# Kernel optimization log

Measured on AMD Instinct MI355X. Metric: run time of the kernel, lower is better.

## Reference

```python
import jax, jax.numpy as jnp
import numpy as np

B, N, DIM, H = 8, 4096, 768, 12
HD = DIM // H
SCALE = HD ** -0.5


def setup_inputs() -> dict:
    key = jax.random.key(0)
    ks = jax.random.split(key, 6)
    x = jax.random.normal(ks[0], (B, N, DIM), dtype=jnp.float32)
    # torch nn.Linear weights: [out_features, in_features]
    Wqkv = jax.random.normal(ks[1], (3 * DIM, DIM), dtype=jnp.float32) * (DIM ** -0.5)
    Wp = jax.random.normal(ks[2], (DIM, DIM), dtype=jnp.float32) * (DIM ** -0.5)
    bp = jnp.zeros((DIM,), dtype=jnp.float32)
    w_q = jax.random.normal(ks[3], (H, HD), dtype=jnp.float32)
    w_k = jax.random.normal(ks[4], (H, HD), dtype=jnp.float32)
    return {"x": x, "Wqkv": Wqkv, "Wp": Wp, "bp": bp, "w_q": w_q, "w_k": w_k}


def reference(x, Wqkv, Wp, bp, w_q, w_k):
    b, n, c = x.shape
    qkv = x @ Wqkv.T                                   # [B,N,3C]
    # rearrange 'B N (qkv H C) -> qkv B H N C'
    qkv = qkv.reshape(b, n, 3, H, HD).transpose(2, 0, 3, 1, 4)
    q, k, v = qkv[0], qkv[1], qkv[2]                   # each [B,H,N,hd]

    alpha = jnp.einsum('bhnc,hc->bhn', q, w_q) * SCALE
    alpha = jax.nn.softmax(alpha, axis=-1)             # [B,H,N]
    global_q = jnp.einsum('bhn,bhnc->bhc', alpha, q)   # [B,H,hd]

    p = global_q[:, :, None, :] * k                    # [B,H,N,hd]
    beta = jnp.einsum('bhnc,hc->bhn', p, w_k) * SCALE
    beta = jax.nn.softmax(beta, axis=-1)
    global_k = jnp.einsum('bhn,bhnc->bhc', beta, k)    # [B,H,hd]

    u = global_k[:, :, None, :] * v                    # [B,H,N,hd]
    q_flat = q.transpose(0, 2, 1, 3).reshape(b, n, c)  # 'B H N C -> B N (H C)'
    u_flat = u.transpose(0, 2, 1, 3).reshape(b, n, c)
    return u_flat @ Wp.T + bp + q_flat
```

## Files before the change

### kernel.cpp

```cpp
#include <hip/hip_runtime.h>
#include <hip/hip_bf16.h>
#include <cstdint>
#include <cstddef>

#define B_ 8
#define N_ 4096
#define DIM_ 768
#define H_ 12
#define M_ (B_*N_)
#define SCALE_ 0.125f
#define NS2 16
#define KDIM 768
#define NKT 12
#define NITER 6
#define QKS 1536

typedef __attribute__((ext_vector_type(8))) short s8v;
typedef __attribute__((ext_vector_type(4))) float f4v;

__device__ inline float bf2f(unsigned short u) {
    unsigned v = ((unsigned)u) << 16;
    return __builtin_bit_cast(float, v);
}
__device__ inline unsigned short f2bf(float f) {
    unsigned u = __builtin_bit_cast(unsigned, f);
    return (unsigned short)((u + 0x7FFFu + ((u >> 16) & 1u)) >> 16);
}
__device__ inline void gload16(const void* g, void* l) {
    __builtin_amdgcn_global_load_lds(
        (const __attribute__((address_space(1))) void*)g,
        (__attribute__((address_space(3))) void*)l, 16, 0, 0);
}

#define BARX() __builtin_amdgcn_s_barrier()
#define PRIO1() __builtin_amdgcn_s_setprio(1)
#define PRIO0() __builtin_amdgcn_s_setprio(0)
#define VM4() asm volatile("s_waitcnt vmcnt(4)" ::: "memory")
#define VM0() asm volatile("s_waitcnt vmcnt(0)" ::: "memory")

template<int EPI>
__global__ __launch_bounds__(512, 2)
void gemm8(const unsigned short* __restrict__ A, int ldaE,
           const unsigned short* __restrict__ Bmat,
           unsigned short* __restrict__ Cb,
           int Nc, int ntn)
{
    __shared__ __align__(16) char smem[131072];
    const int tid = threadIdx.x;
    const int l = tid & 63, w = tid >> 6;
    const int lr = l & 15, g = l >> 4;
    const int wm = w >> 2, wn = w & 3;

    const int nwg = gridDim.x, cpx = nwg >> 3;
    const int bid = blockIdx.x;
    int lg = (bid & 7) * cpx + (bid >> 3);

    size_t batch_off = 0;
    if (EPI == 2) {
        const int bb = lg / 9;
        lg -= bb * 9;
        batch_off = (size_t)bb * (DIM_ * DIM_);
    }
    const int tm = lg / ntn, tn = lg % ntn;
    const int m0 = tm * 256, n0 = tn * 256;

    const long ldaB = (long)ldaE * 2;
    const long ldbB = (long)KDIM * 2;

    const int srA = w * 8 + (l >> 3);
    const int kbs = (l & 7) * 16;
    const int kbx = kbs ^ ((srA & 7) << 4);
    long offA[2], offB[2];
    offA[0] = (long)(srA) * ldaB + kbx;
    offA[1] = (long)(128 + srA) * ldaB + kbx;
    offB[0] = (long)(((srA >> 5)) * 64 + (srA & 31)) * ldbB + kbx;
    offB[1] = (long)((2 + (srA >> 5)) * 64 + (srA & 31)) * ldbB + kbx;

    const char* Abase = (const char*)(A + batch_off + (size_t)m0 * ldaE);
    const char* Bbase = (const char*)(Bmat + (size_t)n0 * KDIM);

    const int aoff = (wm * 64 + lr) * 128;
    const int boff = (wn * 32 + lr) * 128;
    const int kx0 = (g * 16) ^ ((lr & 7) << 4);
    const int kx1 = (64 + g * 16) ^ ((lr & 7) << 4);

    f4v acc[8][4] = {};
    s8v af[4][2];
    s8v bfr[2][2][2];

#define STG_A(buf_, qm_, kt_) { \
    const char* s0_ = Abase + (long)(kt_) * 2 + (long)(qm_) * 64 * ldaB; \
    char* d0_ = smem + ((buf_) * 4 + (qm_)) * 16384 + w * 1024; \
    gload16(s0_ + offA[0], d0_); \
    gload16(s0_ + offA[1], d0_ + 8192); }

#define STG_B(buf_, qn_, kt_) { \
    const char* s0_ = Bbase + (long)(kt_) * 2 + (long)(qn_) * 32 * ldbB; \
    char* d0_ = smem + ((buf_) * 4 + 2 + (qn_)) * 16384 + w * 1024; \
    gload16(s0_ + offB[0], d0_); \
    gload16(s0_ + offB[1], d0_ + 8192); }

#define DS_A(buf_, qm_) { \
    const char* ba_ = smem + ((buf_) * 4 + (qm_)) * 16384 + aoff; \
    af[0][0] = *(const s8v*)(ba_ +    0 + kx0); af[0][1] = *(const s8v*)(ba_ +    0 + kx1); \
    af[1][0] = *(const s8v*)(ba_ + 2048 + kx0); af[1][1] = *(const s8v*)(ba_ + 2048 + kx1); \
    af[2][0] = *(const s8v*)(ba_ + 4096 + kx0); af[2][1] = *(const s8v*)(ba_ + 4096 + kx1); \
    af[3][0] = *(const s8v*)(ba_ + 6144 + kx0); af[3][1] = *(const s8v*)(ba_ + 6144 + kx1); }

#define DS_B(buf_, qn_) { \
    const char* bb_ = smem + ((buf_) * 4 + 2 + (qn_)) * 16384 + boff; \
    bfr[qn_][0][0] = *(const s8v*)(bb_ +    0 + kx0); bfr[qn_][0][1] = *(const s8v*)(bb_ +    0 + kx1); \
    bfr[qn_][1][0] = *(const s8v*)(bb_ + 2048 + kx0); bfr[qn_][1][1] = *(const s8v*)(bb_ + 2048 + kx1); }

#define MM(fmg_, fng_, qn_, kk_) \
    acc[fmg_][fng_] = __builtin_amdgcn_mfma_f32_16x16x32_bf16(af[(fmg_)&3][kk_], bfr[qn_][(fng_)&1][kk_], acc[fmg_][fng_], 0, 0, 0);

#define MFMA8(qm_, qn_, kk_) \
    MM((qm_)*4+0, (qn_)*2+0, qn_, kk_) MM((qm_)*4+0, (qn_)*2+1, qn_, kk_) \
    MM((qm_)*4+1, (qn_)*2+0, qn_, kk_) MM((qm_)*4+1, (qn_)*2+1, qn_, kk_) \
    MM((qm_)*4+2, (qn_)*2+0, qn_, kk_) MM((qm_)*4+2, (qn_)*2+1, qn_, kk_) \
    MM((qm_)*4+3, (qn_)*2+0, qn_, kk_) MM((qm_)*4+3, (qn_)*2+1, qn_, kk_)

#define MFMA16(qm_, qn_) { MFMA8(qm_, qn_, 0) MFMA8(qm_, qn_, 1) }

    STG_A(0, 0, 0); STG_B(0, 0, 0); STG_A(0, 1, 0); STG_B(0, 1, 0);
    STG_A(1, 0, 64); STG_B(1, 0, 64);
    VM4(); BARX();

    for (int i = 0; i < NITER; ++i) {
        const int t1k = (2 * i + 1) * 64, t2k = (2 * i + 2) * 64, t3k = (2 * i + 3) * 64;
        const bool h2 = (2 * i + 2) < NKT, h3 = (2 * i + 3) < NKT;
        const bool last = (i == NITER - 1);
        DS_A(0, 0); DS_B(0, 0); STG_B(1, 1, t1k);
        BARX(); PRIO1(); MFMA16(0, 0); PRIO0(); BARX();
        DS_B(0, 1); STG_A(1, 1, t1k);
        BARX(); PRIO1(); MFMA16(0, 1); PRIO0(); BARX();
        DS_A(0, 1); if (h2) STG_A(0, 0, t2k);
        BARX(); PRIO1(); MFMA16(1, 0); PRIO0(); BARX();
        if (h2) STG_B(0, 0, t2k);
        BARX(); PRIO1(); MFMA16(1, 1); PRIO0();
        if (last) { VM0(); } else { VM4(); }
        BARX();
        DS_A(1, 0); DS_B(1, 0); if (h2) STG_A(0, 1, t2k);
        BARX(); PRIO1(); MFMA16(0, 0); PRIO0(); BARX();
        DS_B(1, 1); if (h2) STG_B(0, 1, t2k);
        BARX(); PRIO1(); MFMA16(0, 1); PRIO0(); BARX();
        DS_A(1, 1); if (h3) STG_A(1, 0, t3k);
        BARX(); PRIO1(); MFMA16(1, 0); PRIO0(); BARX();
        if (h3) STG_B(1, 0, t3k);
        BARX(); PRIO1(); MFMA16(1, 1); PRIO0();
        if (last) { VM0(); } else { VM4(); }
        BARX();
    }

#pragma unroll
    for (int fmg = 0; fmg < 8; ++fmg) {
#pragma unroll
        for (int fng = 0; fng < 4; ++fng) {
            const int col = n0 + wn * 64 + fng * 16 + lr;
#pragma unroll
            for (int r = 0; r < 4; ++r) {
                const int row = m0 + wm * 128 + fmg * 16 + g * 4 + r;
                Cb[batch_off + (size_t)row * Nc + col] = f2bf(acc[fmg][fng][r]);
            }
        }
    }
#undef STG_A
#undef STG_B
#undef DS_A
#undef DS_B
#undef MM
#undef MFMA8
#undef MFMA16
}

__global__ __launch_bounds__(512, 2)
void gemm128_epi(const unsigned short* __restrict__ A, int ldaE,
                 const unsigned short* __restrict__ Bmat,
                 float* __restrict__ Cf,
                 const float* __restrict__ bias, const unsigned short* __restrict__ Qf,
                 int Nc, int ntn)
{
    __shared__ __align__(16) char smem[98304];
    const int tid = threadIdx.x;
    const int l = tid & 63, w = tid >> 6;
    const int lr = l & 15, g = l >> 4;
    const int wm = w >> 2, wn = w & 3;

    const int nwg = gridDim.x, cpx = nwg >> 3;
    const int bid = blockIdx.x;
    const int lg = (bid & 7) * cpx + (bid >> 3);
    const int tm = lg / ntn, tn = lg % ntn;
    const int m0 = tm * 128, n0 = tn * 256;

    const long ldaB = (long)ldaE * 2;
    const long ldbB = (long)KDIM * 2;

    const unsigned short* Bp = Bmat + (size_t)(m0 >> 12) * (DIM_ * DIM_);

    const int srA = w * 8 + (l >> 3);
    const int kbs = (l & 7) * 16;
    const int kbx = kbs ^ ((srA & 7) << 4);
    long offA[2], offB[2];
    offA[0] = (long)(srA) * ldaB + kbx;
    offA[1] = (long)(64 + srA) * ldaB + kbx;
    offB[0] = (long)(((srA >> 5)) * 64 + (srA & 31)) * ldbB + kbx;
    offB[1] = (long)((2 + (srA >> 5)) * 64 + (srA & 31)) * ldbB + kbx;

    const char* Abase = (const char*)(A + (size_t)m0 * ldaE);
    const char* Bbase = (const char*)(Bp + (size_t)n0 * KDIM);

    const int aoff = (wm * 64 + lr) * 128;
    const int boff = (wn * 32 + lr) * 128;
    const int kx0 = (g * 16) ^ ((lr & 7) << 4);
    const int kx1 = (64 + g * 16) ^ ((lr & 7) << 4);

    f4v acc[4][4] = {};
    s8v af[4][2];
    s8v bfr[2][2][2];

#define STG_A1(buf_, kt_) { \
    const char* s0_ = Abase + (long)(kt_) * 2; \
    char* d0_ = smem + ((buf_) * 3) * 16384 + w * 1024; \
    gload16(s0_ + offA[0], d0_); \
    gload16(s0_ + offA[1], d0_ + 8192); }

#define STG_B1(buf_, qn_, kt_) { \
    const char* s0_ = Bbase + (long)(kt_) * 2 + (long)(qn_) * 32 * ldbB; \
    char* d0_ = smem + ((buf_) * 3 + 1 + (qn_)) * 16384 + w * 1024; \
    gload16(s0_ + offB[0], d0_); \
    gload16(s0_ + offB[1], d0_ + 8192); }

#define DS_A1(buf_) { \
    const char* ba_ = smem + ((buf_) * 3) * 16384 + aoff; \
    af[0][0] = *(const s8v*)(ba_ +    0 + kx0); af[0][1] = *(const s8v*)(ba_ +    0 + kx1); \
    af[1][0] = *(const s8v*)(ba_ + 2048 + kx0); af[1][1] = *(const s8v*)(ba_ + 2048 + kx1); \
    af[2][0] = *(const s8v*)(ba_ + 4096 + kx0); af[2][1] = *(const s8v*)(ba_ + 4096 + kx1); \
    af[3][0] = *(const s8v*)(ba_ + 6144 + kx0); af[3][1] = *(const s8v*)(ba_ + 6144 + kx1); }

#define DS_B1(buf_, qn_) { \
    const char* bb_ = smem + ((buf_) * 3 + 1 + (qn_)) * 16384 + boff; \
    bfr[qn_][0][0] = *(const s8v*)(bb_ +    0 + kx0); bfr[qn_][0][1] = *(const s8v*)(bb_ +    0 + kx1); \
    bfr[qn_][1][0] = *(const s8v*)(bb_ + 2048 + kx0); bfr[qn_][1][1] = *(const s8v*)(bb_ + 2048 + kx1); }

#define MM1(fm_, fng_, qn_, kk_) \
    acc[fm_][fng_] = __builtin_amdgcn_mfma_f32_16x16x32_bf16(af[fm_][kk_], bfr[qn_][(fng_)&1][kk_], acc[fm_][fng_], 0, 0, 0);

#define MFMA16_1(qn_, kk_) \
    MM1(0, (qn_)*2+0, qn_, kk_) MM1(0, (qn_)*2+1, qn_, kk_) \
    MM1(1, (qn_)*2+0, qn_, kk_) MM1(1, (qn_)*2+1, qn_, kk_) \
    MM1(2, (qn_)*2+0, qn_, kk_) MM1(2, (qn_)*2+1, qn_, kk_) \
    MM1(3, (qn_)*2+0, qn_, kk_) MM1(3, (qn_)*2+1, qn_, kk_)

#define MFMA32_1(qn_) { MFMA16_1(qn_, 0) MFMA16_1(qn_, 1) }

    STG_A1(0, 0); STG_B1(0, 0, 0); STG_B1(0, 1, 0);
    STG_A1(1, 64); STG_B1(1, 0, 64);
    VM4(); BARX();

    for (int i = 0; i < NITER; ++i) {
        const int t1k = (2 * i + 1) * 64, t2k = (2 * i + 2) * 64, t3k = (2 * i + 3) * 64;
        const bool h2 = (2 * i + 2) < NKT, h3 = (2 * i + 3) < NKT;
        const bool last = (i == NITER - 1);
        DS_A1(0); DS_B1(0, 0); STG_B1(1, 1, t1k);
        BARX(); PRIO1(); MFMA32_1(0); PRIO0(); BARX();
        DS_B1(0, 1); if (h2) { STG_A1(0, t2k); STG_B1(0, 0, t2k); }
        BARX(); PRIO1(); MFMA32_1(1); PRIO0();
        if (last) { VM0(); } else { VM4(); }
        BARX();
        DS_A1(1); DS_B1(1, 0); if (h2) STG_B1(0, 1, t2k);
        BARX(); PRIO1(); MFMA32_1(0); PRIO0(); BARX();
        DS_B1(1, 1); if (h3) { STG_A1(1, t3k); STG_B1(1, 0, t3k); }
        BARX(); PRIO1(); MFMA32_1(1); PRIO0();
        if (last) { VM0(); } else { VM4(); }
        BARX();
    }

#pragma unroll
    for (int fm = 0; fm < 4; ++fm) {
#pragma unroll
        for (int fng = 0; fng < 4; ++fng) {
            const int col = n0 + wn * 64 + fng * 16 + lr;
#pragma unroll
            for (int r = 0; r < 4; ++r) {
                const int row = m0 + wm * 64 + fm * 16 + g * 4 + r;
                Cf[(size_t)row * Nc + col] = acc[fm][fng][r] + bias[col]
                                             + bf2f(Qf[(size_t)row * QKS + col]);
            }
        }
    }
#undef STG_A1
#undef STG_B1
#undef DS_A1
#undef DS_B1
#undef MM1
#undef MFMA16_1
#undef MFMA32_1
}

__global__ __launch_bounds__(256)
void fused_path(const unsigned short* __restrict__ qkv, int col_off,
                const float* __restrict__ vec, int per_bh,
                float* __restrict__ partv, float* __restrict__ partms)
{
    const int bid = blockIdx.x;
    const int bh = bid / NS2, sp = bid % NS2;
    const int b = bh / H_, h = bh % H_;
    const int t = threadIdx.x;
    const int lane8 = t & 7, grp = t >> 3;

    const unsigned short* base = qkv + ((size_t)(b * N_ + sp * 256) * QKS)
                                 + col_off + h * 64 + lane8 * 8;
    const float* wv = vec + (per_bh ? bh * 64 : h * 64) + lane8 * 8;
    float w8[8];
#pragma unroll
    for (int j = 0; j < 8; j++) w8[j] = wv[j];

    float q[8][8];
    float d[8];
#pragma unroll
    for (int pass = 0; pass < 8; ++pass) {
        const int row = pass * 32 + grp;
        s8v q8 = *(const s8v*)(base + (size_t)row * QKS);
        float s = 0.f;
#pragma unroll
        for (int j = 0; j < 8; j++) {
            q[pass][j] = bf2f((unsigned short)q8[j]);
            s += q[pass][j] * w8[j];
        }
        s += __shfl_xor(s, 1); s += __shfl_xor(s, 2); s += __shfl_xor(s, 4);
        d[pass] = s * SCALE_;
    }
    float m = d[0];
#pragma unroll
    for (int pass = 1; pass < 8; ++pass) m = fmaxf(m, d[pass]);
    float ssum = 0.f;
    float a8[8] = {};
#pragma unroll
    for (int pass = 0; pass < 8; ++pass) {
        float e = __expf(d[pass] - m);
        ssum += e;
#pragma unroll
        for (int j = 0; j < 8; j++) a8[j] += e * q[pass][j];
    }

    __shared__ float Lm[32], Ls[32];
    __shared__ float La[32][64];
    if (lane8 == 0) { Lm[grp] = m; Ls[grp] = ssum; }
#pragma unroll
    for (int j = 0; j < 8; j++) La[grp][lane8 * 8 + j] = a8[j];
    __syncthreads();

    if (t < 64) {
        float mstar = Lm[0];
#pragma unroll
        for (int g2 = 1; g2 < 32; ++g2) mstar = fmaxf(mstar, Lm[g2]);
        float sstar = 0.f, v = 0.f;
#pragma unroll
        for (int g2 = 0; g2 < 32; ++g2) {
            float e = __expf(Lm[g2] - mstar);
            sstar += Ls[g2] * e;
            v += La[g2][t] * e;
        }
        partv[(size_t)bid * 64 + t] = v;
        if (t == 0) { partms[bid * 2] = mstar; partms[bid * 2 + 1] = sstar; }
    }
}

__global__ void path_reduce(const float* __restrict__ partv, const float* __restrict__ partms,
                            float* __restrict__ gout,
                            const float* __restrict__ wk, float* __restrict__ bvec)
{
    const int bh = blockIdx.x;
    const int t = threadIdx.x;
    const int h = bh % H_;
    float mstar = partms[(bh * NS2) * 2];
#pragma unroll
    for (int p = 1; p < NS2; ++p) mstar = fmaxf(mstar, partms[(bh * NS2 + p) * 2]);
    float sstar = 0.f, v = 0.f;
#pragma unroll
    for (int p = 0; p < NS2; ++p) {
        float e = __expf(partms[(bh * NS2 + p) * 2] - mstar);
        sstar += partms[(bh * NS2 + p) * 2 + 1] * e;
        v += partv[(size_t)(bh * NS2 + p) * 64 + t] * e;
    }
    float g = v / sstar;
    gout[bh * 64 + t] = g;
    if (wk) bvec[bh * 64 + t] = g * wk[h * 64 + t];
}

__global__ void cvt_all(const float* __restrict__ x, const float* __restrict__ Wqkv,
                        unsigned short* __restrict__ xb, unsigned short* __restrict__ wqkb,
                        unsigned short* __restrict__ wvT,
                        int n4x, int n4xw)
{
    int i = blockIdx.x * 256 + threadIdx.x;
    if (i < n4xw) {
        const float* src; unsigned short* dst; int k;
        if (i < n4x) { src = x; dst = xb; k = i; }
        else { src = Wqkv; dst = wqkb; k = i - n4x; }
        float4 v = ((const float4*)src)[k];
        ushort4 o;
        o.x = f2bf(v.x); o.y = f2bf(v.y); o.z = f2bf(v.z); o.w = f2bf(v.w);
        ((ushort4*)dst)[k] = o;
    } else {
        const int k = i - n4xw;
        const int ii = k % DIM_;
        const int c0 = (k / DIM_) * 4;
        ushort4 o;
        o.x = f2bf(Wqkv[(size_t)(2 * DIM_ + c0 + 0) * DIM_ + ii]);
        o.y = f2bf(Wqkv[(size_t)(2 * DIM_ + c0 + 1) * DIM_ + ii]);
        o.z = f2bf(Wqkv[(size_t)(2 * DIM_ + c0 + 2) * DIM_ + ii]);
        o.w = f2bf(Wqkv[(size_t)(2 * DIM_ + c0 + 3) * DIM_ + ii]);
        *(ushort4*)&wvT[(size_t)ii * DIM_ + c0] = o;
    }
}

__global__ __launch_bounds__(256)
void fold_wp(const float* __restrict__ Wp, const float* __restrict__ gk,
             unsigned short* __restrict__ W2)
{
    int idx = blockIdx.x * 256 + threadIdx.x;
    int e4 = idx * 4;
    int b = (int)((unsigned)e4 / (unsigned)(DIM_ * DIM_));
    int rem = e4 - b * (DIM_ * DIM_);
    int c = rem % DIM_;
    float4 wv = *(const float4*)&Wp[rem];
    const float* gp = &gk[b * DIM_ + c];
    ushort4 o;
    o.x = f2bf(wv.x * gp[0]); o.y = f2bf(wv.y * gp[1]);
    o.z = f2bf(wv.z * gp[2]); o.w = f2bf(wv.w * gp[3]);
    *(ushort4*)&W2[e4] = o;
}

extern "C" void kernel_launch(void* const* d_in, const int* in_sizes, int n_in,
                              void* d_out, int out_size, void* d_ws, size_t ws_size,
                              hipStream_t stream)
{
    const float* x    = (const float*)d_in[0];
    const float* Wqkv = (const float*)d_in[1];
    const float* Wp   = (const float*)d_in[2];
    const float* bp   = (const float*)d_in[3];
    const float* w_q  = (const float*)d_in[4];
    const float* w_k  = (const float*)d_in[5];
    float* out = (float*)d_out;

    constexpr size_t NXB  = (size_t)M_ * DIM_;
    constexpr size_t NWQK = (size_t)2 * DIM_ * DIM_;
    constexpr size_t NWV  = (size_t)DIM_ * DIM_;
    constexpr size_t NQK  = (size_t)M_ * QKS;
    constexpr size_t NW2  = (size_t)B_ * DIM_ * DIM_;

    char* p = (char*)d_ws;
    unsigned short* xb    = (unsigned short*)p; p += NXB * 2;
    unsigned short* wqkb  = (unsigned short*)p; p += NWQK * 2;
    unsigned short* wvT   = (unsigned short*)p; p += NWV * 2;
    unsigned short* qkb   = (unsigned short*)p; p += NQK * 2;
    unsigned short* w2b   = (unsigned short*)p; p += NW2 * 2;
    unsigned short* w3b   = (unsigned short*)p; p += NW2 * 2;
    float* pv1  = (float*)p; p += (size_t)B_ * H_ * NS2 * 64 * 4;
    float* pms1 = (float*)p; p += (size_t)B_ * H_ * NS2 * 2 * 4;
    float* gq   = (float*)p; p += (size_t)B_ * H_ * 64 * 4;
    float* bvec = (float*)p; p += (size_t)B_ * H_ * 64 * 4;
    float* gkv  = (float*)p; p += (size_t)B_ * H_ * 64 * 4;

    constexpr int N4X  = (int)(NXB / 4);
    constexpr int N4XW = N4X + (int)(NWQK / 4);
    constexpr int NTOT = N4XW + (int)(NWV / 4);
    cvt_all<<<NTOT / 256, 256, 0, stream>>>(x, Wqkv, xb, wqkb, wvT, N4X, N4XW);

    gemm8<0><<<128 * 6, 512, 0, stream>>>(xb, DIM_, wqkb, qkb, QKS, 6);

    fused_path<<<B_ * H_ * NS2, 256, 0, stream>>>(qkb, 0, w_q, 0, pv1, pms1);
    path_reduce<<<B_ * H_, 64, 0, stream>>>(pv1, pms1, gq, w_k, bvec);

    fused_path<<<B_ * H_ * NS2, 256, 0, stream>>>(qkb, DIM_, bvec, 1, pv1, pms1);
    path_reduce<<<B_ * H_, 64, 0, stream>>>(pv1, pms1, gkv, nullptr, nullptr);

    fold_wp<<<(int)(NW2 / 4 / 256), 256, 0, stream>>>(Wp, gkv, w2b);

    gemm8<2><<<72, 512, 0, stream>>>(w2b, DIM_, wvT, w3b, DIM_, 3);

    gemm128_epi<<<256 * 3, 512, 0, stream>>>(xb, DIM_, w3b, out, bp, qkb, DIM_, 3);
}
```

Before: 223.3 us.

## Fuse alpha-softmax partial reduction into QKV GEMM epilogue and retile weight-fold GEMM

The QKV GEMM epilogue now computes the per-head q·w_q logits, a local max, exp-sum and the weighted q partial sums directly from the accumulators. It writes 32 partial slices per (batch, head), which removes the separate fused_path pass that re-read Q from memory. path_reduce now takes the partial count as a runtime argument. The batched Wp-fold × WvT GEMM moves from a 72-block 256-tile kernel to a 144-block 128-row-tile variant to use more CUs. The cost is extra shuffles and register pressure in the big GEMM's epilogue.

```diff
diff --git a/kernel.cpp b/kernel.cpp
--- a/kernel.cpp
+++ b/kernel.cpp
@@ -38,11 +38,12 @@
 #define VM4() asm volatile("s_waitcnt vmcnt(4)" ::: "memory")
 #define VM0() asm volatile("s_waitcnt vmcnt(0)" ::: "memory")
 
-template<int EPI>
 __global__ __launch_bounds__(512, 2)
 void gemm8(const unsigned short* __restrict__ A, int ldaE,
            const unsigned short* __restrict__ Bmat,
            unsigned short* __restrict__ Cb,
+           const float* __restrict__ w_q,
+           float* __restrict__ pv1, float* __restrict__ pms1,
            int Nc, int ntn)
 {
     __shared__ __align__(16) char smem[131072];
@@ -53,14 +54,7 @@
 
     const int nwg = gridDim.x, cpx = nwg >> 3;
     const int bid = blockIdx.x;
-    int lg = (bid & 7) * cpx + (bid >> 3);
-
-    size_t batch_off = 0;
-    if (EPI == 2) {
-        const int bb = lg / 9;
-        lg -= bb * 9;
-        batch_off = (size_t)bb * (DIM_ * DIM_);
-    }
+    const int lg = (bid & 7) * cpx + (bid >> 3);
     const int tm = lg / ntn, tn = lg % ntn;
     const int m0 = tm * 256, n0 = tn * 256;
 
@@ -76,7 +70,7 @@
     offB[0] = (long)(((srA >> 5)) * 64 + (srA & 31)) * ldbB + kbx;
     offB[1] = (long)((2 + (srA >> 5)) * 64 + (srA & 31)) * ldbB + kbx;
 
-    const char* Abase = (const char*)(A + batch_off + (size_t)m0 * ldaE);
+    const char* Abase = (const char*)(A + (size_t)m0 * ldaE);
     const char* Bbase = (const char*)(Bmat + (size_t)n0 * KDIM);
 
     const int aoff = (wm * 64 + lr) * 128;
@@ -161,7 +155,66 @@
 #pragma unroll
             for (int r = 0; r < 4; ++r) {
                 const int row = m0 + wm * 128 + fmg * 16 + g * 4 + r;
-                Cb[batch_off + (size_t)row * Nc + col] = f2bf(acc[fmg][fng][r]);
+                Cb[(size_t)row * Nc + col] = f2bf(acc[fmg][fng][r]);
+            }
+        }
+    }
+
+    if (tn < 3) {
+        const int h = tn * 4 + wn;
+        float wq[4];
+#pragma unroll
+        for (int f = 0; f < 4; ++f) wq[f] = w_q[h * 64 + f * 16 + lr];
+
+        float d[8][4];
+#pragma unroll
+        for (int fmg = 0; fmg < 8; ++fmg) {
+#pragma unroll
+            for (int r = 0; r < 4; ++r) {
+                float s = acc[fmg][0][r] * wq[0] + acc[fmg][1][r] * wq[1]
+                        + acc[fmg][2][r] * wq[2] + acc[fmg][3][r] * wq[3];
+                s += __shfl_xor(s, 1); s += __shfl_xor(s, 2);
+                s += __shfl_xor(s, 4); s += __shfl_xor(s, 8);
+                d[fmg][r] = s * SCALE_;
+            }
+        }
+        float mw = d[0][0];
+#pragma unroll
+        for (int fmg = 0; fmg < 8; ++fmg)
+#pragma unroll
+            for (int r = 0; r < 4; ++r) mw = fmaxf(mw, d[fmg][r]);
+        mw = fmaxf(mw, __shfl_xor(mw, 16));
+        mw = fmaxf(mw, __shfl_xor(mw, 32));
+
+        float ssum = 0.f;
+        float pvec[4] = {};
+#pragma unroll
+        for (int fmg = 0; fmg < 8; ++fmg) {
+#pragma unroll
+            for (int r = 0; r < 4; ++r) {
+                const float e = __expf(d[fmg][r] - mw);
+                ssum += e;
+#pragma unroll
+                for (int f = 0; f < 4; ++f) pvec[f] += e * acc[fmg][f][r];
+            }
+        }
+        ssum += __shfl_xor(ssum, 16); ssum += __shfl_xor(ssum, 32);
+#pragma unroll
+        for (int f = 0; f < 4; ++f) {
+            pvec[f] += __shfl_xor(pvec[f], 16);
+            pvec[f] += __shfl_xor(pvec[f], 32);
+        }
+
+        const int b = m0 >> 12;
+        const int bh = b * H_ + h;
+        const int slice = ((m0 & (N_ - 1)) >> 7) + wm;
+        if (g == 0) {
+#pragma unroll
+            for (int f = 0; f < 4; ++f)
+                pv1[(size_t)(bh * 32 + slice) * 64 + f * 16 + lr] = pvec[f];
+            if (lr == 0) {
+                pms1[(bh * 32 + slice) * 2] = mw;
+                pms1[(bh * 32 + slice) * 2 + 1] = ssum;
             }
         }
     }
@@ -174,12 +227,13 @@
 #undef MFMA16
 }
 
+template<int MODE>
 __global__ __launch_bounds__(512, 2)
-void gemm128_epi(const unsigned short* __restrict__ A, int ldaE,
-                 const unsigned short* __restrict__ Bmat,
-                 float* __restrict__ Cf,
-                 const float* __restrict__ bias, const unsigned short* __restrict__ Qf,
-                 int Nc, int ntn)
+void gemm128(const unsigned short* __restrict__ A, int ldaE,
+             const unsigned short* __restrict__ Bmat,
+             float* __restrict__ Cf, unsigned short* __restrict__ CbO,
+             const float* __restrict__ bias, const unsigned short* __restrict__ Qf,
+             int Nc, int ntn)
 {
     __shared__ __align__(16) char smem[98304];
     const int tid = threadIdx.x;
@@ -196,7 +250,8 @@
     const long ldaB = (long)ldaE * 2;
     const long ldbB = (long)KDIM * 2;
 
-    const unsigned short* Bp = Bmat + (size_t)(m0 >> 12) * (DIM_ * DIM_);
+    const unsigned short* Bp = Bmat;
+    if (MODE == 0) Bp = Bmat + (size_t)(m0 >> 12) * (DIM_ * DIM_);
 
     const int srA = w * 8 + (l >> 3);
     const int kbs = (l & 7) * 16;
@@ -284,8 +339,12 @@
 #pragma unroll
             for (int r = 0; r < 4; ++r) {
                 const int row = m0 + wm * 64 + fm * 16 + g * 4 + r;
-                Cf[(size_t)row * Nc + col] = acc[fm][fng][r] + bias[col]
-                                             + bf2f(Qf[(size_t)row * QKS + col]);
+                if (MODE == 0) {
+                    Cf[(size_t)row * Nc + col] = acc[fm][fng][r] + bias[col]
+                                                 + bf2f(Qf[(size_t)row * QKS + col]);
+                } else {
+                    CbO[(size_t)row * Nc + col] = f2bf(acc[fm][fng][r]);
+                }
             }
         }
     }
@@ -368,21 +427,19 @@
 }
 
 __global__ void path_reduce(const float* __restrict__ partv, const float* __restrict__ partms,
-                            float* __restrict__ gout,
+                            int nsp, float* __restrict__ gout,
                             const float* __restrict__ wk, float* __restrict__ bvec)
 {
     const int bh = blockIdx.x;
     const int t = threadIdx.x;
     const int h = bh % H_;
-    float mstar = partms[(bh * NS2) * 2];
-#pragma unroll
-    for (int p = 1; p < NS2; ++p) mstar = fmaxf(mstar, partms[(bh * NS2 + p) * 2]);
+    float mstar = partms[(bh * nsp) * 2];
+    for (int p = 1; p < nsp; ++p) mstar = fmaxf(mstar, partms[(bh * nsp + p) * 2]);
     float sstar = 0.f, v = 0.f;
-#pragma unroll
-    for (int p = 0; p < NS2; ++p) {
-        float e = __expf(partms[(bh * NS2 + p) * 2] - mstar);
-        sstar += partms[(bh * NS2 + p) * 2 + 1] * e;
-        v += partv[(size_t)(bh * NS2 + p) * 64 + t] * e;
+    for (int p = 0; p < nsp; ++p) {
+        float e = __expf(partms[(bh * nsp + p) * 2] - mstar);
+        sstar += partms[(bh * nsp + p) * 2 + 1] * e;
+        v += partv[(size_t)(bh * nsp + p) * 64 + t] * e;
     }
     float g = v / sstar;
     gout[bh * 64 + t] = g;
@@ -458,8 +515,10 @@
     unsigned short* qkb   = (unsigned short*)p; p += NQK * 2;
     unsigned short* w2b   = (unsigned short*)p; p += NW2 * 2;
     unsigned short* w3b   = (unsigned short*)p; p += NW2 * 2;
-    float* pv1  = (float*)p; p += (size_t)B_ * H_ * NS2 * 64 * 4;
-    float* pms1 = (float*)p; p += (size_t)B_ * H_ * NS2 * 2 * 4;
+    float* pv1  = (float*)p; p += (size_t)B_ * H_ * 32 * 64 * 4;
+    float* pms1 = (float*)p; p += (size_t)B_ * H_ * 32 * 2 * 4;
+    float* pv2  = (float*)p; p += (size_t)B_ * H_ * NS2 * 64 * 4;
+    float* pms2 = (float*)p; p += (size_t)B_ * H_ * NS2 * 2 * 4;
     float* gq   = (float*)p; p += (size_t)B_ * H_ * 64 * 4;
     float* bvec = (float*)p; p += (size_t)B_ * H_ * 64 * 4;
     float* gkv  = (float*)p; p += (size_t)B_ * H_ * 64 * 4;
@@ -469,17 +528,17 @@
     constexpr int NTOT = N4XW + (int)(NWV / 4);
     cvt_all<<<NTOT / 256, 256, 0, stream>>>(x, Wqkv, xb, wqkb, wvT, N4X, N4XW);
 
-    gemm8<0><<<128 * 6, 512, 0, stream>>>(xb, DIM_, wqkb, qkb, QKS, 6);
-
-    fused_path<<<B_ * H_ * NS2, 256, 0, stream>>>(qkb, 0, w_q, 0, pv1, pms1);
-    path_reduce<<<B_ * H_, 64, 0, stream>>>(pv1, pms1, gq, w_k, bvec);
-
-    fused_path<<<B_ * H_ * NS2, 256, 0, stream>>>(qkb, DIM_, bvec, 1, pv1, pms1);
-    path_reduce<<<B_ * H_, 64, 0, stream>>>(pv1, pms1, gkv, nullptr, nullptr);
+    gemm8<<<128 * 6, 512, 0, stream>>>(xb, DIM_, wqkb, qkb, w_q, pv1, pms1, QKS, 6);
+
+    path_reduce<<<B_ * H_, 64, 0, stream>>>(pv1, pms1, 32, gq, w_k, bvec);
+
+    fused_path<<<B_ * H_ * NS2, 256, 0, stream>>>(qkb, DIM_, bvec, 1, pv2, pms2);
+    path_reduce<<<B_ * H_, 64, 0, stream>>>(pv2, pms2, NS2, gkv, nullptr, nullptr);
 
     fold_wp<<<(int)(NW2 / 4 / 256), 256, 0, stream>>>(Wp, gkv, w2b);
 
-    gemm8<2><<<72, 512, 0, stream>>>(w2b, DIM_, wvT, w3b, DIM_, 3);
-
-    gemm128_epi<<<256 * 3, 512, 0, stream>>>(xb, DIM_, w3b, out, bp, qkb, DIM_, 3);
-}
+    gemm128<1><<<48 * 3, 512, 0, stream>>>(w2b, DIM_, wvT, nullptr, w3b, nullptr, nullptr,
+                                           DIM_, 3);
+
+    gemm128<0><<<256 * 3, 512, 0, stream>>>(xb, DIM_, w3b, out, nullptr, bp, qkb, DIM_, 3);
+}
```

After: 229.0 us. +2.6%, slower.

## Eliminate QK projection GEMM by folding weights into score vectors and final GEMM

Applied to the files above, without the earlier changes.

Drops the large x@Wqk GEMM that materialized Q and K. Attention scores are computed directly from x against precomputed projected vectors (Wq^T w_q, and per-batch Wk^T(gq*w_k)), and x-weighted sums are reduced back through Wqkv in small reduce kernels. The q_flat residual is folded into the final GEMM weight by adding Wq to the folded Wp*gk*Wv matrix, so the last GEMM only adds bias. This trades a big GEMM and its Q/K buffer traffic for two passes over x, larger fp32 partial buffers, and some bf16 rounding of the combined weights.

```diff
diff --git a/kernel.cpp b/kernel.cpp
--- a/kernel.cpp
+++ b/kernel.cpp
@@ -9,11 +9,9 @@
 #define H_ 12
 #define M_ (B_*N_)
 #define SCALE_ 0.125f
-#define NS2 16
 #define KDIM 768
 #define NKT 12
 #define NITER 6
-#define QKS 1536
 
 typedef __attribute__((ext_vector_type(8))) short s8v;
 typedef __attribute__((ext_vector_type(4))) float f4v;
@@ -36,150 +34,16 @@
 #define PRIO1() __builtin_amdgcn_s_setprio(1)
 #define PRIO0() __builtin_amdgcn_s_setprio(0)
 #define VM4() asm volatile("s_waitcnt vmcnt(4)" ::: "memory")
+#define VM2() asm volatile("s_waitcnt vmcnt(2)" ::: "memory")
 #define VM0() asm volatile("s_waitcnt vmcnt(0)" ::: "memory")
 
-template<int EPI>
+template<int MODE>
 __global__ __launch_bounds__(512, 2)
-void gemm8(const unsigned short* __restrict__ A, int ldaE,
-           const unsigned short* __restrict__ Bmat,
-           unsigned short* __restrict__ Cb,
-           int Nc, int ntn)
-{
-    __shared__ __align__(16) char smem[131072];
-    const int tid = threadIdx.x;
-    const int l = tid & 63, w = tid >> 6;
-    const int lr = l & 15, g = l >> 4;
-    const int wm = w >> 2, wn = w & 3;
-
-    const int nwg = gridDim.x, cpx = nwg >> 3;
-    const int bid = blockIdx.x;
-    int lg = (bid & 7) * cpx + (bid >> 3);
-
-    size_t batch_off = 0;
-    if (EPI == 2) {
-        const int bb = lg / 9;
-        lg -= bb * 9;
-        batch_off = (size_t)bb * (DIM_ * DIM_);
-    }
-    const int tm = lg / ntn, tn = lg % ntn;
-    const int m0 = tm * 256, n0 = tn * 256;
-
-    const long ldaB = (long)ldaE * 2;
-    const long ldbB = (long)KDIM * 2;
-
-    const int srA = w * 8 + (l >> 3);
-    const int kbs = (l & 7) * 16;
-    const int kbx = kbs ^ ((srA & 7) << 4);
-    long offA[2], offB[2];
-    offA[0] = (long)(srA) * ldaB + kbx;
-    offA[1] = (long)(128 + srA) * ldaB + kbx;
-    offB[0] = (long)(((srA >> 5)) * 64 + (srA & 31)) * ldbB + kbx;
-    offB[1] = (long)((2 + (srA >> 5)) * 64 + (srA & 31)) * ldbB + kbx;
-
-    const char* Abase = (const char*)(A + batch_off + (size_t)m0 * ldaE);
-    const char* Bbase = (const char*)(Bmat + (size_t)n0 * KDIM);
-
-    const int aoff = (wm * 64 + lr) * 128;
-    const int boff = (wn * 32 + lr) * 128;
-    const int kx0 = (g * 16) ^ ((lr & 7) << 4);
-    const int kx1 = (64 + g * 16) ^ ((lr & 7) << 4);
-
-    f4v acc[8][4] = {};
-    s8v af[4][2];
-    s8v bfr[2][2][2];
-
-#define STG_A(buf_, qm_, kt_) { \
-    const char* s0_ = Abase + (long)(kt_) * 2 + (long)(qm_) * 64 * ldaB; \
-    char* d0_ = smem + ((buf_) * 4 + (qm_)) * 16384 + w * 1024; \
-    gload16(s0_ + offA[0], d0_); \
-    gload16(s0_ + offA[1], d0_ + 8192); }
-
-#define STG_B(buf_, qn_, kt_) { \
-    const char* s0_ = Bbase + (long)(kt_) * 2 + (long)(qn_) * 32 * ldbB; \
-    char* d0_ = smem + ((buf_) * 4 + 2 + (qn_)) * 16384 + w * 1024; \
-    gload16(s0_ + offB[0], d0_); \
-    gload16(s0_ + offB[1], d0_ + 8192); }
-
-#define DS_A(buf_, qm_) { \
-    const char* ba_ = smem + ((buf_) * 4 + (qm_)) * 16384 + aoff; \
-    af[0][0] = *(const s8v*)(ba_ +    0 + kx0); af[0][1] = *(const s8v*)(ba_ +    0 + kx1); \
-    af[1][0] = *(const s8v*)(ba_ + 2048 + kx0); af[1][1] = *(const s8v*)(ba_ + 2048 + kx1); \
-    af[2][0] = *(const s8v*)(ba_ + 4096 + kx0); af[2][1] = *(const s8v*)(ba_ + 4096 + kx1); \
-    af[3][0] = *(const s8v*)(ba_ + 6144 + kx0); af[3][1] = *(const s8v*)(ba_ + 6144 + kx1); }
-
-#define DS_B(buf_, qn_) { \
-    const char* bb_ = smem + ((buf_) * 4 + 2 + (qn_)) * 16384 + boff; \
-    bfr[qn_][0][0] = *(const s8v*)(bb_ +    0 + kx0); bfr[qn_][0][1] = *(const s8v*)(bb_ +    0 + kx1); \
-    bfr[qn_][1][0] = *(const s8v*)(bb_ + 2048 + kx0); bfr[qn_][1][1] = *(const s8v*)(bb_ + 2048 + kx1); }
-
-#define MM(fmg_, fng_, qn_, kk_) \
-    acc[fmg_][fng_] = __builtin_amdgcn_mfma_f32_16x16x32_bf16(af[(fmg_)&3][kk_], bfr[qn_][(fng_)&1][kk_], acc[fmg_][fng_], 0, 0, 0);
-
-#define MFMA8(qm_, qn_, kk_) \
-    MM((qm_)*4+0, (qn_)*2+0, qn_, kk_) MM((qm_)*4+0, (qn_)*2+1, qn_, kk_) \
-    MM((qm_)*4+1, (qn_)*2+0, qn_, kk_) MM((qm_)*4+1, (qn_)*2+1, qn_, kk_) \
-    MM((qm_)*4+2, (qn_)*2+0, qn_, kk_) MM((qm_)*4+2, (qn_)*2+1, qn_, kk_) \
-    MM((qm_)*4+3, (qn_)*2+0, qn_, kk_) MM((qm_)*4+3, (qn_)*2+1, qn_, kk_)
-
-#define MFMA16(qm_, qn_) { MFMA8(qm_, qn_, 0) MFMA8(qm_, qn_, 1) }
-
-    STG_A(0, 0, 0); STG_B(0, 0, 0); STG_A(0, 1, 0); STG_B(0, 1, 0);
-    STG_A(1, 0, 64); STG_B(1, 0, 64);
-    VM4(); BARX();
-
-    for (int i = 0; i < NITER; ++i) {
-        const int t1k = (2 * i + 1) * 64, t2k = (2 * i + 2) * 64, t3k = (2 * i + 3) * 64;
-        const bool h2 = (2 * i + 2) < NKT, h3 = (2 * i + 3) < NKT;
-        const bool last = (i == NITER - 1);
-        DS_A(0, 0); DS_B(0, 0); STG_B(1, 1, t1k);
-        BARX(); PRIO1(); MFMA16(0, 0); PRIO0(); BARX();
-        DS_B(0, 1); STG_A(1, 1, t1k);
-        BARX(); PRIO1(); MFMA16(0, 1); PRIO0(); BARX();
-        DS_A(0, 1); if (h2) STG_A(0, 0, t2k);
-        BARX(); PRIO1(); MFMA16(1, 0); PRIO0(); BARX();
-        if (h2) STG_B(0, 0, t2k);
-        BARX(); PRIO1(); MFMA16(1, 1); PRIO0();
-        if (last) { VM0(); } else { VM4(); }
-        BARX();
-        DS_A(1, 0); DS_B(1, 0); if (h2) STG_A(0, 1, t2k);
-        BARX(); PRIO1(); MFMA16(0, 0); PRIO0(); BARX();
-        DS_B(1, 1); if (h2) STG_B(0, 1, t2k);
-        BARX(); PRIO1(); MFMA16(0, 1); PRIO0(); BARX();
-        DS_A(1, 1); if (h3) STG_A(1, 0, t3k);
-        BARX(); PRIO1(); MFMA16(1, 0); PRIO0(); BARX();
-        if (h3) STG_B(1, 0, t3k);
-        BARX(); PRIO1(); MFMA16(1, 1); PRIO0();
-        if (last) { VM0(); } else { VM4(); }
-        BARX();
-    }
-
-#pragma unroll
-    for (int fmg = 0; fmg < 8; ++fmg) {
-#pragma unroll
-        for (int fng = 0; fng < 4; ++fng) {
-            const int col = n0 + wn * 64 + fng * 16 + lr;
-#pragma unroll
-            for (int r = 0; r < 4; ++r) {
-                const int row = m0 + wm * 128 + fmg * 16 + g * 4 + r;
-                Cb[batch_off + (size_t)row * Nc + col] = f2bf(acc[fmg][fng][r]);
-            }
-        }
-    }
-#undef STG_A
-#undef STG_B
-#undef DS_A
-#undef DS_B
-#undef MM
-#undef MFMA8
-#undef MFMA16
-}
-
-__global__ __launch_bounds__(512, 2)
-void gemm128_epi(const unsigned short* __restrict__ A, int ldaE,
-                 const unsigned short* __restrict__ Bmat,
-                 float* __restrict__ Cf,
-                 const float* __restrict__ bias, const unsigned short* __restrict__ Qf,
-                 int Nc, int ntn)
+void gemm128(const unsigned short* __restrict__ A, int ldaE,
+             const unsigned short* __restrict__ Bmat,
+             float* __restrict__ Cf, unsigned short* __restrict__ CbO,
+             const float* __restrict__ bias, const float* __restrict__ addW,
+             int Nc, int ntn)
 {
     __shared__ __align__(16) char smem[98304];
     const int tid = threadIdx.x;
@@ -196,7 +60,8 @@
     const long ldaB = (long)ldaE * 2;
     const long ldbB = (long)KDIM * 2;
 
-    const unsigned short* Bp = Bmat + (size_t)(m0 >> 12) * (DIM_ * DIM_);
+    const unsigned short* Bp = Bmat;
+    if (MODE == 0) Bp = Bmat + (size_t)(m0 >> 12) * (DIM_ * DIM_);
 
     const int srA = w * 8 + (l >> 3);
     const int kbs = (l & 7) * 16;
@@ -276,6 +141,7 @@
         BARX();
     }
 
+    const int jb = m0 % DIM_;
 #pragma unroll
     for (int fm = 0; fm < 4; ++fm) {
 #pragma unroll
@@ -283,9 +149,14 @@
             const int col = n0 + wn * 64 + fng * 16 + lr;
 #pragma unroll
             for (int r = 0; r < 4; ++r) {
-                const int row = m0 + wm * 64 + fm * 16 + g * 4 + r;
-                Cf[(size_t)row * Nc + col] = acc[fm][fng][r] + bias[col]
-                                             + bf2f(Qf[(size_t)row * QKS + col]);
+                const int ro = wm * 64 + fm * 16 + g * 4 + r;
+                const int row = m0 + ro;
+                if (MODE == 0) {
+                    Cf[(size_t)row * Nc + col] = acc[fm][fng][r] + bias[col];
+                } else {
+                    CbO[(size_t)row * Nc + col] =
+                        f2bf(acc[fm][fng][r] + addW[(size_t)(jb + ro) * DIM_ + col]);
+                }
             }
         }
     }
@@ -298,113 +169,239 @@
 #undef MFMA32_1
 }
 
+template<int PATH>
+__global__ __launch_bounds__(256, 2)
+void score_sum(const unsigned short* __restrict__ xb,
+               const unsigned short* __restrict__ Vmat,
+               float* __restrict__ svecp,
+               float* __restrict__ pms)
+{
+    const int bid = blockIdx.x;
+    const int b = bid >> 6, sp = bid & 63;
+    const int tid = threadIdx.x;
+    const int l = tid & 63, w = tid >> 6;
+    const int lr = l & 15, g = l >> 4;
+
+    __shared__ __align__(16) char smem[20480];
+    __shared__ float e_lds[64][16];
+    __shared__ float Lm[4][16], Ls[4][16];
+
+    const char* Abase = (const char*)xb + (size_t)(b * N_ + sp * 64) * 1536;
+    const char* Vbase = (const char*)Vmat + (PATH ? (size_t)b * 16 * 1536 : 0);
+
+    const int sw = ((l & 7) * 16) ^ ((l >> 3) << 4);
+
+#define STG(buf_, kt_) { \
+    _Pragma("unroll") \
+    for (int j_ = 0; j_ < 2; ++j_) { \
+        const int rr_ = (w * 2 + j_) * 8 + (l >> 3); \
+        gload16(Abase + (size_t)rr_ * 1536 + (size_t)(kt_) * 2 + sw, \
+                smem + (buf_) * 10240 + (w * 2 + j_) * 1024); } \
+    if (w < 2) { \
+        const int rv_ = w * 8 + (l >> 3); \
+        gload16(Vbase + (size_t)rv_ * 1536 + (size_t)(kt_) * 2 + sw, \
+                smem + (buf_) * 10240 + 8192 + w * 1024); } }
+
+    const int kx0 = (g * 16) ^ ((lr & 7) << 4);
+    const int kx1 = (64 + g * 16) ^ ((lr & 7) << 4);
+
+    f4v acc = {};
+    s8v a0, a1, b0, b1;
+
+    STG(0, 0);
+    for (int kt = 0; kt < 12; ++kt) {
+        if (kt < 11) STG((kt + 1) & 1, (kt + 1) * 64);
+        if (kt == 11) { VM0(); } else { VM2(); }
+        BARX();
+        {
+            const char* ab = smem + (kt & 1) * 10240 + (w * 16 + lr) * 128;
+            const char* vb = smem + (kt & 1) * 10240 + 8192 + lr * 128;
+            a0 = *(const s8v*)(ab + kx0); a1 = *(const s8v*)(ab + kx1);
+            b0 = *(const s8v*)(vb + kx0); b1 = *(const s8v*)(vb + kx1);
+        }
+        acc = __builtin_amdgcn_mfma_f32_16x16x32_bf16(a0, b0, acc, 0, 0, 0);
+        acc = __builtin_amdgcn_mfma_f32_16x16x32_bf16(a1, b1, acc, 0, 0, 0);
+        BARX();
+    }
+#undef STG
+
+    float d[4];
+#pragma unroll
+    for (int r = 0; r < 4; ++r) d[r] = acc[r] * SCALE_;
+
+    float mw = fmaxf(fmaxf(d[0], d[1]), fmaxf(d[2], d[3]));
+    mw = fmaxf(mw, __shfl_xor(mw, 16));
+    mw = fmaxf(mw, __shfl_xor(mw, 32));
+    if (l < 16) Lm[w][lr] = mw;
+    BARX();
+    const float mfin = fmaxf(fmaxf(Lm[0][lr], Lm[1][lr]), fmaxf(Lm[2][lr], Lm[3][lr]));
+
+    float ssum = 0.f;
+#pragma unroll
+    for (int r = 0; r < 4; ++r) {
+        const float e = __expf(d[r] - mfin);
+        ssum += e;
+        e_lds[w * 16 + g * 4 + r][lr] = e;
+    }
+    ssum += __shfl_xor(ssum, 16);
+    ssum += __shfl_xor(ssum, 32);
+    if (l < 16) Ls[w][lr] = ssum;
+    BARX();
+
+    if (tid < 12) {
+        const float m2 = fmaxf(fmaxf(Lm[0][tid], Lm[1][tid]), fmaxf(Lm[2][tid], Lm[3][tid]));
+        const float s2 = Ls[0][tid] + Ls[1][tid] + Ls[2][tid] + Ls[3][tid];
+        pms[((size_t)(b * H_ + tid) * 64 + sp) * 2 + 0] = m2;
+        pms[((size_t)(b * H_ + tid) * 64 + sp) * 2 + 1] = s2;
+    }
+
+    const int hh = tid & 15, dd = tid >> 4;
+    if (hh < 12) {
+        float a48[48] = {};
+        const unsigned short* xp = xb + (size_t)(b * N_ + sp * 64) * 768 + dd * 48;
+        for (int row = 0; row < 64; ++row) {
+            const float e = e_lds[row][hh];
+            const unsigned short* xr = xp + (size_t)row * 768;
+#pragma unroll
+            for (int i = 0; i < 6; ++i) {
+                s8v xv = *(const s8v*)(xr + i * 8);
+#pragma unroll
+                for (int jj = 0; jj < 8; ++jj)
+                    a48[i * 8 + jj] += e * bf2f((unsigned short)xv[jj]);
+            }
+        }
+        float* so = svecp + ((size_t)(b * 64 + sp) * H_ + hh) * 768 + dd * 48;
+#pragma unroll
+        for (int i4 = 0; i4 < 12; ++i4) {
+            float4 v4;
+            v4.x = a48[i4 * 4]; v4.y = a48[i4 * 4 + 1];
+            v4.z = a48[i4 * 4 + 2]; v4.w = a48[i4 * 4 + 3];
+            *(float4*)(so + i4 * 4) = v4;
+        }
+    }
+}
+
 __global__ __launch_bounds__(256)
-void fused_path(const unsigned short* __restrict__ qkv, int col_off,
-                const float* __restrict__ vec, int per_bh,
-                float* __restrict__ partv, float* __restrict__ partms)
-{
-    const int bid = blockIdx.x;
-    const int bh = bid / NS2, sp = bid % NS2;
-    const int b = bh / H_, h = bh % H_;
+void reduce_a(const float* __restrict__ svecp, const float* __restrict__ pms,
+              const float* __restrict__ Wqkv, const float* __restrict__ w_k,
+              unsigned short* __restrict__ bvecs)
+{
+    const int b = blockIdx.x / H_, h = blockIdx.x % H_;
     const int t = threadIdx.x;
-    const int lane8 = t & 7, grp = t >> 3;
-
-    const unsigned short* base = qkv + ((size_t)(b * N_ + sp * 256) * QKS)
-                                 + col_off + h * 64 + lane8 * 8;
-    const float* wv = vec + (per_bh ? bh * 64 : h * 64) + lane8 * 8;
-    float w8[8];
-#pragma unroll
-    for (int j = 0; j < 8; j++) w8[j] = wv[j];
-
-    float q[8][8];
-    float d[8];
-#pragma unroll
-    for (int pass = 0; pass < 8; ++pass) {
-        const int row = pass * 32 + grp;
-        s8v q8 = *(const s8v*)(base + (size_t)row * QKS);
+    __shared__ float Svec[768];
+    __shared__ float ew[64];
+    __shared__ float gqwk[64];
+
+    const float* pp = pms + (size_t)(b * H_ + h) * 64 * 2;
+    float M = -1e30f;
+    for (int p = 0; p < 64; ++p) M = fmaxf(M, pp[p * 2]);
+    if (t < 64) ew[t] = __expf(pp[t * 2] - M);
+    __syncthreads();
+    float S = 0.f;
+    for (int p = 0; p < 64; ++p) S += ew[p] * pp[p * 2 + 1];
+    const float invS = 1.f / S;
+
+#pragma unroll
+    for (int j = 0; j < 3; ++j) {
+        const int dcol = t + j * 256;
+        float v = 0.f;
+        for (int p = 0; p < 64; ++p)
+            v += ew[p] * svecp[((size_t)(b * 64 + p) * H_ + h) * 768 + dcol];
+        Svec[dcol] = v * invS;
+    }
+    __syncthreads();
+
+    if (t < 64) {
+        const float* wr = Wqkv + (size_t)(h * 64 + t) * 768;
         float s = 0.f;
-#pragma unroll
-        for (int j = 0; j < 8; j++) {
-            q[pass][j] = bf2f((unsigned short)q8[j]);
-            s += q[pass][j] * w8[j];
-        }
-        s += __shfl_xor(s, 1); s += __shfl_xor(s, 2); s += __shfl_xor(s, 4);
-        d[pass] = s * SCALE_;
-    }
-    float m = d[0];
-#pragma unroll
-    for (int pass = 1; pass < 8; ++pass) m = fmaxf(m, d[pass]);
-    float ssum = 0.f;
-    float a8[8] = {};
-#pragma unroll
-    for (int pass = 0; pass < 8; ++pass) {
-        float e = __expf(d[pass] - m);
-        ssum += e;
-#pragma unroll
-        for (int j = 0; j < 8; j++) a8[j] += e * q[pass][j];
-    }
-
-    __shared__ float Lm[32], Ls[32];
-    __shared__ float La[32][64];
-    if (lane8 == 0) { Lm[grp] = m; Ls[grp] = ssum; }
-#pragma unroll
-    for (int j = 0; j < 8; j++) La[grp][lane8 * 8 + j] = a8[j];
+        for (int dcol = 0; dcol < 768; ++dcol) s += wr[dcol] * Svec[dcol];
+        gqwk[t] = s * w_k[h * 64 + t];
+    }
+    __syncthreads();
+
+#pragma unroll
+    for (int j = 0; j < 3; ++j) {
+        const int dcol = t + j * 256;
+        float bv = 0.f;
+        for (int c = 0; c < 64; ++c)
+            bv += gqwk[c] * Wqkv[(size_t)(DIM_ + h * 64 + c) * 768 + dcol];
+        bvecs[(size_t)(b * 16 + h) * 768 + dcol] = f2bf(bv);
+        if (h < 4) bvecs[(size_t)(b * 16 + 12 + h) * 768 + dcol] = 0;
+    }
+}
+
+__global__ __launch_bounds__(256)
+void reduce_b(const float* __restrict__ svecp, const float* __restrict__ pms,
+              const float* __restrict__ Wqkv, float* __restrict__ gkv)
+{
+    const int b = blockIdx.x / H_, h = blockIdx.x % H_;
+    const int t = threadIdx.x;
+    __shared__ float Svec[768];
+    __shared__ float ew[64];
+
+    const float* pp = pms + (size_t)(b * H_ + h) * 64 * 2;
+    float M = -1e30f;
+    for (int p = 0; p < 64; ++p) M = fmaxf(M, pp[p * 2]);
+    if (t < 64) ew[t] = __expf(pp[t * 2] - M);
+    __syncthreads();
+    float S = 0.f;
+    for (int p = 0; p < 64; ++p) S += ew[p] * pp[p * 2 + 1];
+    const float invS = 1.f / S;
+
+#pragma unroll
+    for (int j = 0; j < 3; ++j) {
+        const int dcol = t + j * 256;
+        float v = 0.f;
+        for (int p = 0; p < 64; ++p)
+            v += ew[p] * svecp[((size_t)(b * 64 + p) * H_ + h) * 768 + dcol];
+        Svec[dcol] = v * invS;
+    }
     __syncthreads();
 
     if (t < 64) {
-        float mstar = Lm[0];
-#pragma unroll
-        for (int g2 = 1; g2 < 32; ++g2) mstar = fmaxf(mstar, Lm[g2]);
-        float sstar = 0.f, v = 0.f;
-#pragma unroll
-        for (int g2 = 0; g2 < 32; ++g2) {
-            float e = __expf(Lm[g2] - mstar);
-            sstar += Ls[g2] * e;
-            v += La[g2][t] * e;
-        }
-        partv[(size_t)bid * 64 + t] = v;
-        if (t == 0) { partms[bid * 2] = mstar; partms[bid * 2 + 1] = sstar; }
-    }
-}
-
-__global__ void path_reduce(const float* __restrict__ partv, const float* __restrict__ partms,
-                            float* __restrict__ gout,
-                            const float* __restrict__ wk, float* __restrict__ bvec)
-{
-    const int bh = blockIdx.x;
+        const float* wr = Wqkv + (size_t)(DIM_ + h * 64 + t) * 768;
+        float s = 0.f;
+        for (int dcol = 0; dcol < 768; ++dcol) s += wr[dcol] * Svec[dcol];
+        gkv[b * DIM_ + h * 64 + t] = s;
+    }
+}
+
+__global__ __launch_bounds__(256)
+void avec_prep(const float* __restrict__ Wqkv, const float* __restrict__ w_q,
+               unsigned short* __restrict__ avecb)
+{
+    const int h = blockIdx.x;
     const int t = threadIdx.x;
-    const int h = bh % H_;
-    float mstar = partms[(bh * NS2) * 2];
-#pragma unroll
-    for (int p = 1; p < NS2; ++p) mstar = fmaxf(mstar, partms[(bh * NS2 + p) * 2]);
-    float sstar = 0.f, v = 0.f;
-#pragma unroll
-    for (int p = 0; p < NS2; ++p) {
-        float e = __expf(partms[(bh * NS2 + p) * 2] - mstar);
-        sstar += partms[(bh * NS2 + p) * 2 + 1] * e;
-        v += partv[(size_t)(bh * NS2 + p) * 64 + t] * e;
-    }
-    float g = v / sstar;
-    gout[bh * 64 + t] = g;
-    if (wk) bvec[bh * 64 + t] = g * wk[h * 64 + t];
+    if (h >= H_) {
+#pragma unroll
+        for (int j = 0; j < 3; ++j) avecb[(size_t)h * 768 + t + j * 256] = 0;
+        return;
+    }
+    __shared__ float wl[64];
+    if (t < 64) wl[t] = w_q[h * 64 + t];
+    __syncthreads();
+#pragma unroll
+    for (int j = 0; j < 3; ++j) {
+        const int dcol = t + j * 256;
+        float a = 0.f;
+        for (int c = 0; c < 64; ++c)
+            a += wl[c] * Wqkv[(size_t)(h * 64 + c) * 768 + dcol];
+        avecb[(size_t)h * 768 + dcol] = f2bf(a);
+    }
 }
 
 __global__ void cvt_all(const float* __restrict__ x, const float* __restrict__ Wqkv,
-                        unsigned short* __restrict__ xb, unsigned short* __restrict__ wqkb,
-                        unsigned short* __restrict__ wvT,
-                        int n4x, int n4xw)
+                        unsigned short* __restrict__ xb, unsigned short* __restrict__ wvT,
+                        int n4x)
 {
     int i = blockIdx.x * 256 + threadIdx.x;
-    if (i < n4xw) {
-        const float* src; unsigned short* dst; int k;
-        if (i < n4x) { src = x; dst = xb; k = i; }
-        else { src = Wqkv; dst = wqkb; k = i - n4x; }
-        float4 v = ((const float4*)src)[k];
+    if (i < n4x) {
+        float4 v = ((const float4*)x)[i];
         ushort4 o;
         o.x = f2bf(v.x); o.y = f2bf(v.y); o.z = f2bf(v.z); o.w = f2bf(v.w);
-        ((ushort4*)dst)[k] = o;
+        ((ushort4*)xb)[i] = o;
     } else {
-        const int k = i - n4xw;
+        const int k = i - n4x;
         const int ii = k % DIM_;
         const int c0 = (k / DIM_) * 4;
         ushort4 o;
@@ -445,41 +442,42 @@
     const float* w_k  = (const float*)d_in[5];
     float* out = (float*)d_out;
 
-    constexpr size_t NXB  = (size_t)M_ * DIM_;
-    constexpr size_t NWQK = (size_t)2 * DIM_ * DIM_;
-    constexpr size_t NWV  = (size_t)DIM_ * DIM_;
-    constexpr size_t NQK  = (size_t)M_ * QKS;
-    constexpr size_t NW2  = (size_t)B_ * DIM_ * DIM_;
+    constexpr size_t NXB = (size_t)M_ * DIM_;
+    constexpr size_t NWV = (size_t)DIM_ * DIM_;
+    constexpr size_t NW2 = (size_t)B_ * DIM_ * DIM_;
 
     char* p = (char*)d_ws;
     unsigned short* xb    = (unsigned short*)p; p += NXB * 2;
-    unsigned short* wqkb  = (unsigned short*)p; p += NWQK * 2;
     unsigned short* wvT   = (unsigned short*)p; p += NWV * 2;
-    unsigned short* qkb   = (unsigned short*)p; p += NQK * 2;
     unsigned short* w2b   = (unsigned short*)p; p += NW2 * 2;
-    unsigned short* w3b   = (unsigned short*)p; p += NW2 * 2;
-    float* pv1  = (float*)p; p += (size_t)B_ * H_ * NS2 * 64 * 4;
-    float* pms1 = (float*)p; p += (size_t)B_ * H_ * NS2 * 2 * 4;
-    float* gq   = (float*)p; p += (size_t)B_ * H_ * 64 * 4;
-    float* bvec = (float*)p; p += (size_t)B_ * H_ * 64 * 4;
-    float* gkv  = (float*)p; p += (size_t)B_ * H_ * 64 * 4;
+    unsigned short* w4b   = (unsigned short*)p; p += NW2 * 2;
+    unsigned short* avecb = (unsigned short*)p; p += (size_t)16 * 768 * 2;
+    unsigned short* bvecs = (unsigned short*)p; p += (size_t)B_ * 16 * 768 * 2;
+    float* svecpA = (float*)p; p += (size_t)B_ * 64 * H_ * 768 * 4;
+    float* svecpB = (float*)p; p += (size_t)B_ * 64 * H_ * 768 * 4;
+    float* pmsA   = (float*)p; p += (size_t)B_ * H_ * 64 * 2 * 4;
+    float* pmsB   = (float*)p; p += (size_t)B_ * H_ * 64 * 2 * 4;
+    float* gkv    = (float*)p; p += (size_t)B_ * DIM_ * 4;
 
     constexpr int N4X  = (int)(NXB / 4);
-    constexpr int N4XW = N4X + (int)(NWQK / 4);
-    constexpr int NTOT = N4XW + (int)(NWV / 4);
-    cvt_all<<<NTOT / 256, 256, 0, stream>>>(x, Wqkv, xb, wqkb, wvT, N4X, N4XW);
-
-    gemm8<0><<<128 * 6, 512, 0, stream>>>(xb, DIM_, wqkb, qkb, QKS, 6);
-
-    fused_path<<<B_ * H_ * NS2, 256, 0, stream>>>(qkb, 0, w_q, 0, pv1, pms1);
-    path_reduce<<<B_ * H_, 64, 0, stream>>>(pv1, pms1, gq, w_k, bvec);
-
-    fused_path<<<B_ * H_ * NS2, 256, 0, stream>>>(qkb, DIM_, bvec, 1, pv1, pms1);
-    path_reduce<<<B_ * H_, 64, 0, stream>>>(pv1, pms1, gkv, nullptr, nullptr);
+    constexpr int NTOT = N4X + (int)(NWV / 4);
+    cvt_all<<<NTOT / 256, 256, 0, stream>>>(x, Wqkv, xb, wvT, N4X);
+
+    avec_prep<<<16, 256, 0, stream>>>(Wqkv, w_q, avecb);
+
+    score_sum<0><<<B_ * 64, 256, 0, stream>>>(xb, avecb, svecpA, pmsA);
+
+    reduce_a<<<B_ * H_, 256, 0, stream>>>(svecpA, pmsA, Wqkv, w_k, bvecs);
+
+    score_sum<1><<<B_ * 64, 256, 0, stream>>>(xb, bvecs, svecpB, pmsB);
+
+    reduce_b<<<B_ * H_, 256, 0, stream>>>(svecpB, pmsB, Wqkv, gkv);
 
     fold_wp<<<(int)(NW2 / 4 / 256), 256, 0, stream>>>(Wp, gkv, w2b);
 
-    gemm8<2><<<72, 512, 0, stream>>>(w2b, DIM_, wvT, w3b, DIM_, 3);
-
-    gemm128_epi<<<256 * 3, 512, 0, stream>>>(xb, DIM_, w3b, out, bp, qkb, DIM_, 3);
-}
+    gemm128<1><<<48 * 3, 512, 0, stream>>>(w2b, DIM_, wvT, nullptr, w4b, nullptr, Wqkv,
+                                           DIM_, 3);
+
+    gemm128<0><<<256 * 3, 512, 0, stream>>>(xb, DIM_, w4b, out, nullptr, bp, nullptr,
+                                            DIM_, 3);
+}
```

Measured after the change: 378.7 us. 69.6% more time.
